# Kernel tuning notes

Measured on AMD Instinct MI355X. Metric: run time of the kernel, lower is better.

Reference implementation:

```python
import jax, jax.numpy as jnp
import numpy as np
from functools import partial

OBS, LATENT, HID = 32, 256, 1024


def setup_inputs() -> dict:
    key = jax.random.key(0)
    ks = jax.random.split(key, 16)
    s = 0.05  # small init keeps tanh/relu activations in a healthy range
    B, T = 128, 256
    inp = {
        "y": jax.random.normal(ks[0], (B, T, OBS), dtype=jnp.float32),
        "horizon": 512,
        # tanh-RNN cell params (torch nn.RNN layout: W_ih [H,I], W_hh [H,H])
        "W_ih": jax.random.normal(ks[1], (LATENT, OBS), dtype=jnp.float32) * s,
        "W_hh": jax.random.normal(ks[2], (LATENT, LATENT), dtype=jnp.float32) * s,
        "b_ih": jax.random.normal(ks[3], (LATENT,), dtype=jnp.float32) * s,
        "b_hh": jax.random.normal(ks[4], (LATENT,), dtype=jnp.float32) * s,
        # psi: 5-layer MLP latent -> hid -> hid -> hid -> hid -> obs
        "W1": jax.random.normal(ks[5], (HID, LATENT), dtype=jnp.float32) * s,
        "b1": jnp.zeros((HID,), dtype=jnp.float32),
        "W2": jax.random.normal(ks[6], (HID, HID), dtype=jnp.float32) * s,
        "b2": jnp.zeros((HID,), dtype=jnp.float32),
        "W3": jax.random.normal(ks[7], (HID, HID), dtype=jnp.float32) * s,
        "b3": jnp.zeros((HID,), dtype=jnp.float32),
        "W4": jax.random.normal(ks[8], (HID, HID), dtype=jnp.float32) * s,
        "b4": jnp.zeros((HID,), dtype=jnp.float32),
        "W5": jax.random.normal(ks[9], (OBS, HID), dtype=jnp.float32) * s,
        "b5": jnp.zeros((OBS,), dtype=jnp.float32),
    }
    return inp


def _psi(z, W1, b1, W2, b2, W3, b3, W4, b4, W5, b5):
    h = jax.nn.relu(z @ W1.T + b1)
    h = jax.nn.relu(h @ W2.T + b2)
    h = jax.nn.relu(h @ W3.T + b3)
    h = jax.nn.relu(h @ W4.T + b4)
    return h @ W5.T + b5  # (B, OBS)


def reference(y, horizon, W_ih, W_hh, b_ih, b_hh,
              W1, b1, W2, b2, W3, b3, W4, b4, W5, b5):
    B, T, S = y.shape
    psi = partial(_psi, W1=W1, b1=b1, W2=W2, b2=b2, W3=W3, b3=b3,
                  W4=W4, b4=b4, W5=W5, b5=b5)

    def cell(z, inp):
        return jnp.tanh(inp @ W_ih.T + b_ih + z @ W_hh.T + b_hh)

    z0 = jnp.zeros((B, y.shape[2]), dtype=y.dtype) if False else jnp.zeros((B, W_hh.shape[0]), dtype=y.dtype)

    # Phase 1: teacher-forced. y_hat[t] = psi(z_t) BEFORE consuming y[:, t].
    def step_tf(z, y_t):
        yh = psi(z)
        return cell(z, y_t), yh

    z, yh1 = jax.lax.scan(step_tf, z0, jnp.swapaxes(y, 0, 1))  # yh1: (T,B,S)

    def step_ar(z, _):
        yh = psi(z)
        return cell(z, yh), yh

    z, yh2 = jax.lax.scan(step_ar, z, None, length=horizon - T)  # (H-T,B,S)

    y_hat = jnp.concatenate([yh1, yh2], axis=0)  # (H,B,S)
    return jnp.swapaxes(y_hat, 0, 1)  # (B,H,S)
```

## Files before the change

### kernel.cpp

```cpp
#include <hip/hip_runtime.h>
#include <stdint.h>


#define BATCH 128
#define TTF   256
#define HOR   512
#define OBS   32
#define LAT   256
#define HID   1024

#define GROUPS  8
#define MEMBERS 32
#define ARBLOCKS (GROUPS * MEMBERS)
#define ARTHREADS 128

typedef __attribute__((ext_vector_type(8))) short short8;
typedef __attribute__((ext_vector_type(4))) float floatx4;

#define OFF_WB1   ((size_t)0)
#define OFF_WB2   (OFF_WB1 + (size_t)HID*LAT*2)
#define OFF_WB3   (OFF_WB2 + (size_t)HID*HID*2)
#define OFF_WB4   (OFF_WB3 + (size_t)HID*HID*2)
#define OFF_WB5   (OFF_WB4 + (size_t)HID*HID*2)
#define OFF_CB    (OFF_WB5 + (size_t)OBS*HID*2)
#define OFF_WHH2  (OFF_CB + (size_t)LAT*4)
#define OFF_WIH2  (OFF_WHH2 + (size_t)64*256*8)
#define OFF_ZF    (OFF_WIH2 + (size_t)8*256*8)
#define OFF_Z     (OFF_ZF + (size_t)BATCH*LAT*4)
#define OFF_WBC   (OFF_Z + (size_t)BATCH*TTF*LAT*2)
#define OFF_HB    (OFF_WBC + (size_t)LAT*288*2)
#define OFF_CTR   (OFF_HB + (size_t)GROUPS*8*16*HID*2)
#define OFF_END   (OFF_CTR + (size_t)GROUPS*512)

__device__ __forceinline__ uint16_t f2bf(float f) {
    uint32_t u = __float_as_uint(f);
    u += 0x7fffu + ((u >> 16) & 1u);
    return (uint16_t)(u >> 16);
}
__device__ __forceinline__ float bflo(uint32_t u) { return __uint_as_float(u << 16); }
__device__ __forceinline__ float bfhi(uint32_t u) { return __uint_as_float(u & 0xffff0000u); }

__device__ __forceinline__ float fast_tanh(float x) {
    float ax = fabsf(x);
    float e  = __expf(-2.f * ax);
    float r  = (1.f - e) / (1.f + e);
    return copysignf(r, x);
}

__device__ __forceinline__ int hswz(int row, int col) {
    return row * 1024 + ((((col >> 3) ^ (row & 7)) << 3) | (col & 7));
}
__device__ __forceinline__ int zswz(int row, int col) {
    return row * 256 + ((((col >> 3) ^ (row & 7)) << 3) | (col & 7));
}

__device__ __forceinline__ void st16_mall(void* p, floatx4 v) {
    asm volatile("global_store_dwordx4 %0, %1, off sc0 sc1"
                 :: "v"(p), "v"(v) : "memory");
}

typedef const __attribute__((address_space(1))) void* gas_t;
typedef __attribute__((address_space(3))) void* las_t;
__device__ __forceinline__ void gl_lds16(const void* g, void* l) {
    __builtin_amdgcn_global_load_lds((gas_t)g, (las_t)l, 16, 0, 0x11);
}

__device__ __forceinline__ void stage_h(const uint16_t* src, uint16_t* dst,
                                        int w, int L) {
    const char* gp = (const char*)src + w * 16384 + L * 16;
    char* lp = (char*)dst + w * 16384;
    #pragma unroll
    for (int i = 0; i < 16; i++)
        gl_lds16(gp + i * 1024, lp + i * 1024);
}

__device__ __forceinline__ void gbar(unsigned* ctr, unsigned target) {
    asm volatile("s_waitcnt vmcnt(0)" ::: "memory");
    __syncthreads();
    if (threadIdx.x == 0) {
        __hip_atomic_fetch_add(ctr, 1u, __ATOMIC_RELAXED, __HIP_MEMORY_SCOPE_AGENT);
        while (__hip_atomic_load(ctr, __ATOMIC_RELAXED, __HIP_MEMORY_SCOPE_AGENT) < target) {}
    }
    __syncthreads();
}

__global__ void k_cvt(const float* __restrict__ s, uint16_t* __restrict__ d, int n) {
    int i = blockIdx.x * 256 + threadIdx.x;
    if (i < n) d[i] = f2bf(s[i]);
}

__global__ void k_cb(const float* __restrict__ a, const float* __restrict__ b,
                     float* __restrict__ c) {
    int j = threadIdx.x;
    c[j] = a[j] + b[j];
}

__global__ void k_pack(const float* __restrict__ w, uint2* __restrict__ dst, int klen) {
    int k4 = blockIdx.x, j = threadIdx.x;
    int k = k4 * 4;
    uint32_t a = f2bf(w[(size_t)j * klen + k + 0]);
    uint32_t b = f2bf(w[(size_t)j * klen + k + 1]);
    uint32_t c = f2bf(w[(size_t)j * klen + k + 2]);
    uint32_t d = f2bf(w[(size_t)j * klen + k + 3]);
    uint2 r; r.x = a | (b << 16); r.y = c | (d << 16);
    dst[k4 * 256 + j] = r;
}

__global__ void k_packc(const float* __restrict__ whh, const float* __restrict__ wih,
                        uint16_t* __restrict__ wbc) {
    int col = blockIdx.x;
    for (int k = threadIdx.x; k < 288; k += 256) {
        float v = (k < 256) ? whh[(size_t)col * 256 + k] : wih[(size_t)col * 32 + (k - 256)];
        wbc[(size_t)col * 288 + k] = f2bf(v);
    }
}

__global__ __launch_bounds__(256) void k_rnn_tf(
    const float* __restrict__ y, const uint2* __restrict__ whh2,
    const uint2* __restrict__ wih2, const float* __restrict__ cb,
    uint16_t* __restrict__ Zg, float* __restrict__ zfinal)
{
    __shared__ alignas(16) float zl[LAT];
    __shared__ alignas(16) float ys[OBS];
    int j = threadIdx.x, b = blockIdx.x;
    zl[j] = 0.f;
    __syncthreads();
    const float4* z4 = (const float4*)zl;
    const float4* y4 = (const float4*)ys;
    for (int t = 0; t < TTF; t++) {
        if (j < OBS) ys[j] = y[(size_t)b * (TTF * OBS) + t * OBS + j];
        Zg[((size_t)b * TTF + t) * LAT + j] = f2bf(zl[j]);
        __syncthreads();
        float acc = cb[j];
        #pragma unroll 8
        for (int k4 = 0; k4 < 64; k4++) {
            uint2 wv = whh2[k4 * 256 + j];
            float4 zq = z4[k4];
            acc += bflo(wv.x) * zq.x + bfhi(wv.x) * zq.y
                 + bflo(wv.y) * zq.z + bfhi(wv.y) * zq.w;
        }
        #pragma unroll
        for (int k4 = 0; k4 < 8; k4++) {
            uint2 wv = wih2[k4 * 256 + j];
            float4 yq = y4[k4];
            acc += bflo(wv.x) * yq.x + bfhi(wv.x) * yq.y
                 + bflo(wv.y) * yq.z + bfhi(wv.y) * yq.w;
        }
        __syncthreads();
        zl[j] = fast_tanh(acc);
    }
    __syncthreads();
    zfinal[(size_t)b * LAT + j] = zl[j];
}

__global__ __launch_bounds__(512) void k_psi_bulk(
    const uint16_t* __restrict__ Zg,
    const uint16_t* __restrict__ wb1, const uint16_t* __restrict__ wb2,
    const uint16_t* __restrict__ wb3, const uint16_t* __restrict__ wb4,
    const uint16_t* __restrict__ wb5,
    const float* __restrict__ b1, const float* __restrict__ b2,
    const float* __restrict__ b3, const float* __restrict__ b4,
    const float* __restrict__ b5, float* __restrict__ out)
{
    __shared__ uint16_t hbuf[32 * 1024];
    int tid = threadIdx.x;
    int w = tid >> 6, L = tid & 63, lm = L & 15, q = L >> 4;
    int rb = blockIdx.x * 32;
    int colbase = w * 128;
    floatx4 acc[2][8];
    const floatx4 zero = {0.f, 0.f, 0.f, 0.f};

    #pragma unroll
    for (int mt = 0; mt < 2; mt++)
        #pragma unroll
        for (int nt = 0; nt < 8; nt++) acc[mt][nt] = zero;
    for (int kc = 0; kc < 8; kc++) {
        short8 a0 = *(const short8*)(Zg + (size_t)(rb + lm) * LAT + kc * 32 + q * 8);
        short8 a1 = *(const short8*)(Zg + (size_t)(rb + 16 + lm) * LAT + kc * 32 + q * 8);
        #pragma unroll
        for (int nt = 0; nt < 8; nt++) {
            int n = colbase + nt * 16 + lm;
            short8 bf = *(const short8*)(wb1 + (size_t)n * LAT + kc * 32 + q * 8);
            acc[0][nt] = __builtin_amdgcn_mfma_f32_16x16x32_bf16(a0, bf, acc[0][nt], 0, 0, 0);
            acc[1][nt] = __builtin_amdgcn_mfma_f32_16x16x32_bf16(a1, bf, acc[1][nt], 0, 0, 0);
        }
    }
    #pragma unroll
    for (int mt = 0; mt < 2; mt++)
        #pragma unroll
        for (int nt = 0; nt < 8; nt++) {
            int col = colbase + nt * 16 + lm;
            float bias = b1[col];
            #pragma unroll
            for (int i = 0; i < 4; i++) {
                int row = mt * 16 + q * 4 + i;
                hbuf[hswz(row, col)] = f2bf(fmaxf(acc[mt][nt][i] + bias, 0.f));
            }
        }
    __syncthreads();

    const uint16_t* wbs[3] = {wb2, wb3, wb4};
    const float*    bbs[3] = {b2, b3, b4};
    for (int ll = 0; ll < 3; ll++) {
        const uint16_t* wb = wbs[ll];
        const float* bb = bbs[ll];
        #pragma unroll
        for (int mt = 0; mt < 2; mt++)
            #pragma unroll
            for (int nt = 0; nt < 8; nt++) acc[mt][nt] = zero;
        for (int kc = 0; kc < 32; kc++) {
            int g = ((kc * 4 + q) ^ (lm & 7)) << 3;
            short8 a0 = *(const short8*)(hbuf + lm * 1024 + g);
            short8 a1 = *(const short8*)(hbuf + (16 + lm) * 1024 + g);
            #pragma unroll
            for (int nt = 0; nt < 8; nt++) {
                int n = colbase + nt * 16 + lm;
                short8 bf = *(const short8*)(wb + (size_t)n * HID + kc * 32 + q * 8);
                acc[0][nt] = __builtin_amdgcn_mfma_f32_16x16x32_bf16(a0, bf, acc[0][nt], 0, 0, 0);
                acc[1][nt] = __builtin_amdgcn_mfma_f32_16x16x32_bf16(a1, bf, acc[1][nt], 0, 0, 0);
            }
        }
        __syncthreads();
        #pragma unroll
        for (int mt = 0; mt < 2; mt++)
            #pragma unroll
            for (int nt = 0; nt < 8; nt++) {
                int col = colbase + nt * 16 + lm;
                float bias = bb[col];
                #pragma unroll
                for (int i = 0; i < 4; i++) {
                    int row = mt * 16 + q * 4 + i;
                    hbuf[hswz(row, col)] = f2bf(fmaxf(acc[mt][nt][i] + bias, 0.f));
                }
            }
        __syncthreads();
    }

    if (w < 4) {
        int mt = w >> 1;
        int nb = (w & 1) * 16;
        floatx4 a5 = zero;
        for (int kc = 0; kc < 32; kc++) {
            int g = ((kc * 4 + q) ^ (lm & 7)) << 3;
            short8 a = *(const short8*)(hbuf + (mt * 16 + lm) * 1024 + g);
            short8 bf = *(const short8*)(wb5 + (size_t)(nb + lm) * HID + kc * 32 + q * 8);
            a5 = __builtin_amdgcn_mfma_f32_16x16x32_bf16(a, bf, a5, 0, 0, 0);
        }
        int col = nb + lm;
        float bias = b5[col];
        #pragma unroll
        for (int i = 0; i < 4; i++) {
            int row = mt * 16 + q * 4 + i;
            int r = rb + row;
            int bb_ = r >> 8, tt = r & 255;
            out[(size_t)bb_ * (HOR * OBS) + tt * OBS + col] = a5[i] + bias;
        }
    }
}

__global__ __launch_bounds__(ARTHREADS) void k_ar2(
    const float* __restrict__ zfinal,
    const uint16_t* __restrict__ wb1, const uint16_t* __restrict__ wb2,
    const uint16_t* __restrict__ wb3, const uint16_t* __restrict__ wb4,
    const uint16_t* __restrict__ wb5, const uint16_t* __restrict__ wbc,
    const float* __restrict__ b1g, const float* __restrict__ b2g,
    const float* __restrict__ b3g, const float* __restrict__ b4g,
    const float* __restrict__ b5g, const float* __restrict__ cb,
    uint16_t* __restrict__ hb_all, unsigned* __restrict__ ctr_all,
    float* __restrict__ out)
{
    __shared__ alignas(16) uint16_t hstg[16 * 1024];
    __shared__ alignas(16) uint16_t zst[2 * 16 * 256];
    __shared__ alignas(16) uint16_t yscr[16 * 32];
    __shared__ alignas(16) uint16_t hsl[16 * 32];

    const int tid = threadIdx.x;
    const int g = blockIdx.x >> 5, m = blockIdx.x & 31;
    const int w = tid >> 6, L = tid & 63, lm = L & 15, q = L >> 4, lm7 = lm & 7;
    const int colbase = m * 32;
    const int cl = w * 16 + lm;
    const int rb = g * 16;
    uint16_t* hb = hb_all + (size_t)g * (8 * 16 * HID);
    unsigned* ctr = ctr_all + g * 128;
    const floatx4 zero = {0.f, 0.f, 0.f, 0.f};

    for (int idx = tid; idx < 16 * 256; idx += ARTHREADS) {
        int r = idx >> 8, c = idx & 255;
        zst[zswz(r, c)] = f2bf(zfinal[(size_t)(rb + r) * LAT + c]);
    }
    __syncthreads();
    unsigned tgt = 0;

    #define PUBLISH(DST) do {                                               \
        __syncthreads();                                                    \
        if (tid < 64) {                                                     \
            int row_ = tid >> 2, gr_ = tid & 3;                             \
            floatx4 vv_ = *(const floatx4*)((const char*)hsl + tid * 16);   \
            int gsw_ = (m * 4 + gr_) ^ (row_ & 7);                          \
            st16_mall((char*)(DST) + row_ * 2048 + gsw_ * 16, vv_);         \
        }                                                                   \
        gbar(ctr, tgt += MEMBERS);                                          \
    } while (0)

    #define MID_LAYER(HSRC, HDST, WB, BG) do {                               \
        stage_h(HSRC, hstg, w, L);                                           \
        __syncthreads();                                                     \
        floatx4 acc_ = zero;                                                 \
        const uint16_t* bb_ = WB + (size_t)(colbase + cl) * HID + q * 8;     \
        _Pragma("unroll 8")                                                  \
        for (int kc = 0; kc < 32; kc++) {                                    \
            int gh = (kc * 4 + q) ^ lm7;                                     \
            short8 a_ = *(const short8*)(hstg + lm * 1024 + gh * 8);         \
            short8 b_ = *(const short8*)(bb_ + kc * 32);                     \
            acc_ = __builtin_amdgcn_mfma_f32_16x16x32_bf16(a_, b_, acc_, 0, 0, 0); \
        }                                                                    \
        float bias_ = BG[colbase + cl];                                      \
        _Pragma("unroll")                                                    \
        for (int i = 0; i < 4; i++)                                          \
            hsl[(q * 4 + i) * 32 + cl] = f2bf(fmaxf(acc_[i] + bias_, 0.f));  \
        PUBLISH(HDST);                                                       \
    } while (0)

    #pragma unroll 1
    for (int t = 0; t < HOR - TTF; t++) {
        uint16_t* zcur = zst + (t & 1) * (16 * 256);
        uint16_t* znx  = zst + ((t + 1) & 1) * (16 * 256);
        uint16_t* hp = hb + (t & 1) * (4 * 16 * HID);
        uint16_t* h1 = hp;
        uint16_t* h2 = hp + 16 * HID;
        uint16_t* h3 = hp + 2 * 16 * HID;
        uint16_t* h4 = hp + 3 * 16 * HID;

        {
            floatx4 acc = zero;
            const uint16_t* bb = wb1 + (size_t)(colbase + cl) * LAT + q * 8;
            #pragma unroll
            for (int kc = 0; kc < 8; kc++) {
                int gz = (kc * 4 + q) ^ lm7;
                short8 a = *(const short8*)(zcur + lm * 256 + gz * 8);
                short8 b = *(const short8*)(bb + kc * 32);
                acc = __builtin_amdgcn_mfma_f32_16x16x32_bf16(a, b, acc, 0, 0, 0);
            }
            float bias = b1g[colbase + cl];
            #pragma unroll
            for (int i = 0; i < 4; i++)
                hsl[(q * 4 + i) * 32 + cl] = f2bf(fmaxf(acc[i] + bias, 0.f));
        }
        PUBLISH(h1);

        MID_LAYER(h1, h2, wb2, b2g);
        MID_LAYER(h2, h3, wb3, b3g);
        MID_LAYER(h3, h4, wb4, b4g);

        stage_h(h4, hstg, w, L);
        __syncthreads();
        {
            floatx4 a5 = zero;
            const uint16_t* bb = wb5 + (size_t)cl * HID + q * 8;
            #pragma unroll 8
            for (int kc = 0; kc < 32; kc++) {
                int gh = (kc * 4 + q) ^ lm7;
                short8 a = *(const short8*)(hstg + lm * 1024 + gh * 8);
                short8 b = *(const short8*)(bb + kc * 32);
                a5 = __builtin_amdgcn_mfma_f32_16x16x32_bf16(a, b, a5, 0, 0, 0);
            }
            float bias = b5g[cl];
            float vout[4];
            #pragma unroll
            for (int i = 0; i < 4; i++) {
                float v = a5[i] + bias;
                vout[i] = v;
                yscr[(q * 4 + i) * 32 + cl] = f2bf(v);
            }
            if (m == 0) {
                #pragma unroll
                for (int i = 0; i < 4; i++)
                    out[(size_t)(rb + q * 4 + i) * (HOR * OBS) + (TTF + t) * OBS + cl] = vout[i];
            }
        }
        __syncthreads();
        #pragma unroll 1
        for (int ct = 0; ct < 8; ct++) {
            int ccol = w * 128 + ct * 16 + lm;
            floatx4 cc = zero;
            const uint16_t* bb2 = wbc + (size_t)ccol * 288 + q * 8;
            #pragma unroll
            for (int kc = 0; kc < 9; kc++) {
                short8 a;
                if (kc < 8) {
                    int gz = (kc * 4 + q) ^ lm7;
                    a = *(const short8*)(zcur + lm * 256 + gz * 8);
                } else {
                    a = *(const short8*)(yscr + lm * 32 + q * 8);
                }
                short8 b = *(const short8*)(bb2 + kc * 32);
                cc = __builtin_amdgcn_mfma_f32_16x16x32_bf16(a, b, cc, 0, 0, 0);
            }
            float cbv = cb[ccol];
            #pragma unroll
            for (int i = 0; i < 4; i++)
                znx[zswz(q * 4 + i, ccol)] = f2bf(fast_tanh(cc[i] + cbv));
        }
        __syncthreads();
    }
    #undef MID_LAYER
    #undef PUBLISH
}

extern "C" void kernel_launch(void* const* d_in, const int* in_sizes, int n_in,
                              void* d_out, int out_size, void* d_ws, size_t ws_size,
                              hipStream_t stream) {
    (void)in_sizes; (void)n_in; (void)out_size; (void)ws_size;
    const float* y    = (const float*)d_in[0];
    const float* W_ih = (const float*)d_in[2];
    const float* W_hh = (const float*)d_in[3];
    const float* b_ih = (const float*)d_in[4];
    const float* b_hh = (const float*)d_in[5];
    const float* W1   = (const float*)d_in[6];
    const float* b1   = (const float*)d_in[7];
    const float* W2   = (const float*)d_in[8];
    const float* b2   = (const float*)d_in[9];
    const float* W3   = (const float*)d_in[10];
    const float* b3   = (const float*)d_in[11];
    const float* W4   = (const float*)d_in[12];
    const float* b4   = (const float*)d_in[13];
    const float* W5   = (const float*)d_in[14];
    const float* b5   = (const float*)d_in[15];
    float* out = (float*)d_out;
    char* ws = (char*)d_ws;

    uint16_t* WB1  = (uint16_t*)(ws + OFF_WB1);
    uint16_t* WB2  = (uint16_t*)(ws + OFF_WB2);
    uint16_t* WB3  = (uint16_t*)(ws + OFF_WB3);
    uint16_t* WB4  = (uint16_t*)(ws + OFF_WB4);
    uint16_t* WB5  = (uint16_t*)(ws + OFF_WB5);
    float*    CB   = (float*)(ws + OFF_CB);
    uint2*    WHH2 = (uint2*)(ws + OFF_WHH2);
    uint2*    WIH2 = (uint2*)(ws + OFF_WIH2);
    float*    ZF   = (float*)(ws + OFF_ZF);
    uint16_t* Zbuf = (uint16_t*)(ws + OFF_Z);
    uint16_t* WBC  = (uint16_t*)(ws + OFF_WBC);
    uint16_t* HB   = (uint16_t*)(ws + OFF_HB);
    unsigned* CTR  = (unsigned*)(ws + OFF_CTR);

    k_cvt<<<(HID*LAT + 255) / 256, 256, 0, stream>>>(W1, WB1, HID * LAT);
    k_cvt<<<(HID*HID + 255) / 256, 256, 0, stream>>>(W2, WB2, HID * HID);
    k_cvt<<<(HID*HID + 255) / 256, 256, 0, stream>>>(W3, WB3, HID * HID);
    k_cvt<<<(HID*HID + 255) / 256, 256, 0, stream>>>(W4, WB4, HID * HID);
    k_cvt<<<(OBS*HID + 255) / 256, 256, 0, stream>>>(W5, WB5, OBS * HID);
    k_cb<<<1, 256, 0, stream>>>(b_ih, b_hh, CB);
    k_pack<<<64, 256, 0, stream>>>(W_hh, WHH2, LAT);
    k_pack<<<8, 256, 0, stream>>>(W_ih, WIH2, OBS);
    k_packc<<<256, 256, 0, stream>>>(W_hh, W_ih, WBC);
    hipMemsetAsync(CTR, 0, GROUPS * 512, stream);

    k_rnn_tf<<<BATCH, 256, 0, stream>>>(y, WHH2, WIH2, CB, Zbuf, ZF);

    k_psi_bulk<<<(BATCH * TTF) / 32, 512, 0, stream>>>(
        Zbuf, WB1, WB2, WB3, WB4, WB5, b1, b2, b3, b4, b5, out);

    void* args[] = {
        (void*)&ZF, (void*)&WB1, (void*)&WB2, (void*)&WB3, (void*)&WB4,
        (void*)&WB5, (void*)&WBC, (void*)&b1, (void*)&b2, (void*)&b3,
        (void*)&b4, (void*)&b5, (void*)&CB, (void*)&HB, (void*)&CTR,
        (void*)&out
    };
    hipError_t ce = hipLaunchCooperativeKernel((const void*)k_ar2,
                                               dim3(ARBLOCKS), dim3(ARTHREADS),
                                               args, 0, stream);
    if (ce != hipSuccess) {
        (void)hipGetLastError();
        k_ar2<<<dim3(ARBLOCKS), dim3(ARTHREADS), 0, stream>>>(
            ZF, WB1, WB2, WB3, WB4, WB5, WBC, b1, b2, b3, b4, b5, CB,
            HB, CTR, out);
    }
}
```

Measured before the change: 7.373 ms.

## Fuse bulk psi into AR kernel and replace counter barrier with per-layer flags

Merges the teacher-forced psi MLP blocks into the autoregressive kernel as extra blocks, so the bulk psi work can run alongside the latency-bound AR recurrence instead of before it. Replaces the atomic-counter group barrier with per-member epoch flags per layer, polled in parallel across a wavefront, to cut synchronisation latency. It drops the cooperative launch, so AR blocks depend on being co-resident while 2048 psi blocks compete for CUs, which risks delay or deadlock if AR blocks are not scheduled first.

```diff
diff --git a/kernel.cpp b/kernel.cpp
--- a/kernel.cpp
+++ b/kernel.cpp
@@ -12,6 +12,8 @@
 #define GROUPS  8
 #define MEMBERS 32
 #define ARBLOCKS (GROUPS * MEMBERS)
+#define PSIBLKS  2048
+#define FUSEDBLKS (ARBLOCKS + PSIBLKS)
 #define ARTHREADS 128
 
 typedef __attribute__((ext_vector_type(8))) short short8;
@@ -72,16 +74,6 @@
     #pragma unroll
     for (int i = 0; i < 16; i++)
         gl_lds16(gp + i * 1024, lp + i * 1024);
-}
-
-__device__ __forceinline__ void gbar(unsigned* ctr, unsigned target) {
-    asm volatile("s_waitcnt vmcnt(0)" ::: "memory");
-    __syncthreads();
-    if (threadIdx.x == 0) {
-        __hip_atomic_fetch_add(ctr, 1u, __ATOMIC_RELAXED, __HIP_MEMORY_SCOPE_AGENT);
-        while (__hip_atomic_load(ctr, __ATOMIC_RELAXED, __HIP_MEMORY_SCOPE_AGENT) < target) {}
-    }
-    __syncthreads();
 }
 
 __global__ void k_cvt(const float* __restrict__ s, uint16_t* __restrict__ d, int n) {
@@ -153,113 +145,8 @@
     zfinal[(size_t)b * LAT + j] = zl[j];
 }
 
-__global__ __launch_bounds__(512) void k_psi_bulk(
-    const uint16_t* __restrict__ Zg,
-    const uint16_t* __restrict__ wb1, const uint16_t* __restrict__ wb2,
-    const uint16_t* __restrict__ wb3, const uint16_t* __restrict__ wb4,
-    const uint16_t* __restrict__ wb5,
-    const float* __restrict__ b1, const float* __restrict__ b2,
-    const float* __restrict__ b3, const float* __restrict__ b4,
-    const float* __restrict__ b5, float* __restrict__ out)
-{
-    __shared__ uint16_t hbuf[32 * 1024];
-    int tid = threadIdx.x;
-    int w = tid >> 6, L = tid & 63, lm = L & 15, q = L >> 4;
-    int rb = blockIdx.x * 32;
-    int colbase = w * 128;
-    floatx4 acc[2][8];
-    const floatx4 zero = {0.f, 0.f, 0.f, 0.f};
-
-    #pragma unroll
-    for (int mt = 0; mt < 2; mt++)
-        #pragma unroll
-        for (int nt = 0; nt < 8; nt++) acc[mt][nt] = zero;
-    for (int kc = 0; kc < 8; kc++) {
-        short8 a0 = *(const short8*)(Zg + (size_t)(rb + lm) * LAT + kc * 32 + q * 8);
-        short8 a1 = *(const short8*)(Zg + (size_t)(rb + 16 + lm) * LAT + kc * 32 + q * 8);
-        #pragma unroll
-        for (int nt = 0; nt < 8; nt++) {
-            int n = colbase + nt * 16 + lm;
-            short8 bf = *(const short8*)(wb1 + (size_t)n * LAT + kc * 32 + q * 8);
-            acc[0][nt] = __builtin_amdgcn_mfma_f32_16x16x32_bf16(a0, bf, acc[0][nt], 0, 0, 0);
-            acc[1][nt] = __builtin_amdgcn_mfma_f32_16x16x32_bf16(a1, bf, acc[1][nt], 0, 0, 0);
-        }
-    }
-    #pragma unroll
-    for (int mt = 0; mt < 2; mt++)
-        #pragma unroll
-        for (int nt = 0; nt < 8; nt++) {
-            int col = colbase + nt * 16 + lm;
-            float bias = b1[col];
-            #pragma unroll
-            for (int i = 0; i < 4; i++) {
-                int row = mt * 16 + q * 4 + i;
-                hbuf[hswz(row, col)] = f2bf(fmaxf(acc[mt][nt][i] + bias, 0.f));
-            }
-        }
-    __syncthreads();
-
-    const uint16_t* wbs[3] = {wb2, wb3, wb4};
-    const float*    bbs[3] = {b2, b3, b4};
-    for (int ll = 0; ll < 3; ll++) {
-        const uint16_t* wb = wbs[ll];
-        const float* bb = bbs[ll];
-        #pragma unroll
-        for (int mt = 0; mt < 2; mt++)
-            #pragma unroll
-            for (int nt = 0; nt < 8; nt++) acc[mt][nt] = zero;
-        for (int kc = 0; kc < 32; kc++) {
-            int g = ((kc * 4 + q) ^ (lm & 7)) << 3;
-            short8 a0 = *(const short8*)(hbuf + lm * 1024 + g);
-            short8 a1 = *(const short8*)(hbuf + (16 + lm) * 1024 + g);
-            #pragma unroll
-            for (int nt = 0; nt < 8; nt++) {
-                int n = colbase + nt * 16 + lm;
-                short8 bf = *(const short8*)(wb + (size_t)n * HID + kc * 32 + q * 8);
-                acc[0][nt] = __builtin_amdgcn_mfma_f32_16x16x32_bf16(a0, bf, acc[0][nt], 0, 0, 0);
-                acc[1][nt] = __builtin_amdgcn_mfma_f32_16x16x32_bf16(a1, bf, acc[1][nt], 0, 0, 0);
-            }
-        }
-        __syncthreads();
-        #pragma unroll
-        for (int mt = 0; mt < 2; mt++)
-            #pragma unroll
-            for (int nt = 0; nt < 8; nt++) {
-                int col = colbase + nt * 16 + lm;
-                float bias = bb[col];
-                #pragma unroll
-                for (int i = 0; i < 4; i++) {
-                    int row = mt * 16 + q * 4 + i;
-                    hbuf[hswz(row, col)] = f2bf(fmaxf(acc[mt][nt][i] + bias, 0.f));
-                }
-            }
-        __syncthreads();
-    }
-
-    if (w < 4) {
-        int mt = w >> 1;
-        int nb = (w & 1) * 16;
-        floatx4 a5 = zero;
-        for (int kc = 0; kc < 32; kc++) {
-            int g = ((kc * 4 + q) ^ (lm & 7)) << 3;
-            short8 a = *(const short8*)(hbuf + (mt * 16 + lm) * 1024 + g);
-            short8 bf = *(const short8*)(wb5 + (size_t)(nb + lm) * HID + kc * 32 + q * 8);
-            a5 = __builtin_amdgcn_mfma_f32_16x16x32_bf16(a, bf, a5, 0, 0, 0);
-        }
-        int col = nb + lm;
-        float bias = b5[col];
-        #pragma unroll
-        for (int i = 0; i < 4; i++) {
-            int row = mt * 16 + q * 4 + i;
-            int r = rb + row;
-            int bb_ = r >> 8, tt = r & 255;
-            out[(size_t)bb_ * (HOR * OBS) + tt * OBS + col] = a5[i] + bias;
-        }
-    }
-}
-
-__global__ __launch_bounds__(ARTHREADS) void k_ar2(
-    const float* __restrict__ zfinal,
+__global__ __launch_bounds__(ARTHREADS) void k_fused(
+    const float* __restrict__ zfinal, const uint16_t* __restrict__ Zg,
     const uint16_t* __restrict__ wb1, const uint16_t* __restrict__ wb2,
     const uint16_t* __restrict__ wb3, const uint16_t* __restrict__ wb4,
     const uint16_t* __restrict__ wb5, const uint16_t* __restrict__ wbc,
@@ -275,36 +162,126 @@
     __shared__ alignas(16) uint16_t hsl[16 * 32];
 
     const int tid = threadIdx.x;
+    const int w = tid >> 6, L = tid & 63, lm = L & 15, q = L >> 4, lm7 = lm & 7;
+    const floatx4 zero = {0.f, 0.f, 0.f, 0.f};
+
+    if (blockIdx.x >= ARBLOCKS) {
+        const int p = blockIdx.x - ARBLOCKS;
+        const int rb2 = p * 16;
+        floatx4 acc[2][16];
+
+        #pragma unroll
+        for (int h = 0; h < 2; h++)
+            #pragma unroll
+            for (int nt = 0; nt < 16; nt++) acc[h][nt] = zero;
+        for (int kc = 0; kc < 8; kc++) {
+            short8 a0 = *(const short8*)(Zg + (size_t)(rb2 + lm) * LAT + kc * 32 + q * 8);
+            #pragma unroll
+            for (int h = 0; h < 2; h++)
+                #pragma unroll
+                for (int nt = 0; nt < 16; nt++) {
+                    int n = w * 512 + h * 256 + nt * 16 + lm;
+                    short8 bf = *(const short8*)(wb1 + (size_t)n * LAT + kc * 32 + q * 8);
+                    acc[h][nt] = __builtin_amdgcn_mfma_f32_16x16x32_bf16(a0, bf, acc[h][nt], 0, 0, 0);
+                }
+        }
+        #pragma unroll
+        for (int h = 0; h < 2; h++)
+            #pragma unroll
+            for (int nt = 0; nt < 16; nt++) {
+                int col = w * 512 + h * 256 + nt * 16 + lm;
+                float bias = b1g[col];
+                #pragma unroll
+                for (int i = 0; i < 4; i++)
+                    hstg[hswz(q * 4 + i, col)] = f2bf(fmaxf(acc[h][nt][i] + bias, 0.f));
+            }
+        __syncthreads();
+
+        for (int ll = 0; ll < 3; ll++) {
+            const uint16_t* wb = (ll == 0) ? wb2 : (ll == 1) ? wb3 : wb4;
+            const float* bb = (ll == 0) ? b2g : (ll == 1) ? b3g : b4g;
+            #pragma unroll
+            for (int h = 0; h < 2; h++)
+                #pragma unroll
+                for (int nt = 0; nt < 16; nt++) acc[h][nt] = zero;
+            for (int kc = 0; kc < 32; kc++) {
+                short8 a0 = *(const short8*)(hstg + lm * 1024 + (((kc * 4 + q) ^ lm7) << 3));
+                #pragma unroll
+                for (int h = 0; h < 2; h++)
+                    #pragma unroll
+                    for (int nt = 0; nt < 16; nt++) {
+                        int n = w * 512 + h * 256 + nt * 16 + lm;
+                        short8 bf = *(const short8*)(wb + (size_t)n * HID + kc * 32 + q * 8);
+                        acc[h][nt] = __builtin_amdgcn_mfma_f32_16x16x32_bf16(a0, bf, acc[h][nt], 0, 0, 0);
+                    }
+            }
+            __syncthreads();
+            #pragma unroll
+            for (int h = 0; h < 2; h++)
+                #pragma unroll
+                for (int nt = 0; nt < 16; nt++) {
+                    int col = w * 512 + h * 256 + nt * 16 + lm;
+                    float bias = bb[col];
+                    #pragma unroll
+                    for (int i = 0; i < 4; i++)
+                        hstg[hswz(q * 4 + i, col)] = f2bf(fmaxf(acc[h][nt][i] + bias, 0.f));
+                }
+            __syncthreads();
+        }
+
+        floatx4 a5 = zero;
+        for (int kc = 0; kc < 32; kc++) {
+            short8 a = *(const short8*)(hstg + lm * 1024 + (((kc * 4 + q) ^ lm7) << 3));
+            short8 bf = *(const short8*)(wb5 + (size_t)(w * 16 + lm) * HID + kc * 32 + q * 8);
+            a5 = __builtin_amdgcn_mfma_f32_16x16x32_bf16(a, bf, a5, 0, 0, 0);
+        }
+        int col = w * 16 + lm;
+        float bias = b5g[col];
+        #pragma unroll
+        for (int i = 0; i < 4; i++) {
+            int r = rb2 + q * 4 + i;
+            out[(size_t)(r >> 8) * (HOR * OBS) + (r & 255) * OBS + col] = a5[i] + bias;
+        }
+        return;
+    }
+
     const int g = blockIdx.x >> 5, m = blockIdx.x & 31;
-    const int w = tid >> 6, L = tid & 63, lm = L & 15, q = L >> 4, lm7 = lm & 7;
     const int colbase = m * 32;
     const int cl = w * 16 + lm;
     const int rb = g * 16;
     uint16_t* hb = hb_all + (size_t)g * (8 * 16 * HID);
-    unsigned* ctr = ctr_all + g * 128;
-    const floatx4 zero = {0.f, 0.f, 0.f, 0.f};
+    unsigned* flg = ctr_all + g * 128;
 
     for (int idx = tid; idx < 16 * 256; idx += ARTHREADS) {
         int r = idx >> 8, c = idx & 255;
         zst[zswz(r, c)] = f2bf(zfinal[(size_t)(rb + r) * LAT + c]);
     }
     __syncthreads();
-    unsigned tgt = 0;
-
-    #define PUBLISH(DST) do {                                               \
-        __syncthreads();                                                    \
-        if (tid < 64) {                                                     \
-            int row_ = tid >> 2, gr_ = tid & 3;                             \
-            floatx4 vv_ = *(const floatx4*)((const char*)hsl + tid * 16);   \
-            int gsw_ = (m * 4 + gr_) ^ (row_ & 7);                          \
-            st16_mall((char*)(DST) + row_ * 2048 + gsw_ * 16, vv_);         \
-        }                                                                   \
-        gbar(ctr, tgt += MEMBERS);                                          \
+
+    #define EXCHANGE(DST, FL, EP) do {                                       \
+        __syncthreads();                                                     \
+        if (tid < 64) {                                                      \
+            int row_ = tid >> 2, gr_ = tid & 3;                              \
+            floatx4 vv_ = *(const floatx4*)((const char*)hsl + tid * 16);    \
+            int gsw_ = (m * 4 + gr_) ^ (row_ & 7);                           \
+            st16_mall((char*)(DST) + row_ * 2048 + gsw_ * 16, vv_);          \
+            asm volatile("s_waitcnt vmcnt(0)" ::: "memory");                 \
+            if (tid == 0)                                                    \
+                __hip_atomic_store(flg + (FL) * 32 + m, (EP),                \
+                                   __ATOMIC_RELAXED, __HIP_MEMORY_SCOPE_AGENT); \
+        }                                                                    \
+        {                                                                    \
+            unsigned* fp_ = flg + (FL) * 32 + (L & 31);                      \
+            unsigned v_;                                                     \
+            do {                                                             \
+                v_ = __hip_atomic_load(fp_, __ATOMIC_RELAXED,                \
+                                       __HIP_MEMORY_SCOPE_AGENT);            \
+            } while (!__all((int)(v_ >= (EP))));                             \
+            asm volatile("" ::: "memory");                                   \
+        }                                                                    \
     } while (0)
 
-    #define MID_LAYER(HSRC, HDST, WB, BG) do {                               \
-        stage_h(HSRC, hstg, w, L);                                           \
-        __syncthreads();                                                     \
+    #define MID_COMPUTE(WB, BG) do {                                         \
         floatx4 acc_ = zero;                                                 \
         const uint16_t* bb_ = WB + (size_t)(colbase + cl) * HID + q * 8;     \
         _Pragma("unroll 8")                                                  \
@@ -318,11 +295,11 @@
         _Pragma("unroll")                                                    \
         for (int i = 0; i < 4; i++)                                          \
             hsl[(q * 4 + i) * 32 + cl] = f2bf(fmaxf(acc_[i] + bias_, 0.f));  \
-        PUBLISH(HDST);                                                       \
     } while (0)
 
     #pragma unroll 1
     for (int t = 0; t < HOR - TTF; t++) {
+        const unsigned ep = (unsigned)(t + 1);
         uint16_t* zcur = zst + (t & 1) * (16 * 256);
         uint16_t* znx  = zst + ((t + 1) & 1) * (16 * 256);
         uint16_t* hp = hb + (t & 1) * (4 * 16 * HID);
@@ -346,14 +323,25 @@
             for (int i = 0; i < 4; i++)
                 hsl[(q * 4 + i) * 32 + cl] = f2bf(fmaxf(acc[i] + bias, 0.f));
         }
-        PUBLISH(h1);
-
-        MID_LAYER(h1, h2, wb2, b2g);
-        MID_LAYER(h2, h3, wb3, b3g);
-        MID_LAYER(h3, h4, wb4, b4g);
-
+        EXCHANGE(h1, 0, ep);
+        stage_h(h1, hstg, w, L);
+        __syncthreads();
+
+        MID_COMPUTE(wb2, b2g);
+        EXCHANGE(h2, 1, ep);
+        stage_h(h2, hstg, w, L);
+        __syncthreads();
+
+        MID_COMPUTE(wb3, b3g);
+        EXCHANGE(h3, 2, ep);
+        stage_h(h3, hstg, w, L);
+        __syncthreads();
+
+        MID_COMPUTE(wb4, b4g);
+        EXCHANGE(h4, 3, ep);
         stage_h(h4, hstg, w, L);
         __syncthreads();
+
         {
             floatx4 a5 = zero;
             const uint16_t* bb = wb5 + (size_t)cl * HID + q * 8;
@@ -403,8 +391,8 @@
         }
         __syncthreads();
     }
-    #undef MID_LAYER
-    #undef PUBLISH
+    #undef MID_COMPUTE
+    #undef EXCHANGE
 }
 
 extern "C" void kernel_launch(void* const* d_in, const int* in_sizes, int n_in,
@@ -456,22 +444,7 @@
 
     k_rnn_tf<<<BATCH, 256, 0, stream>>>(y, WHH2, WIH2, CB, Zbuf, ZF);
 
-    k_psi_bulk<<<(BATCH * TTF) / 32, 512, 0, stream>>>(
-        Zbuf, WB1, WB2, WB3, WB4, WB5, b1, b2, b3, b4, b5, out);
-
-    void* args[] = {
-        (void*)&ZF, (void*)&WB1, (void*)&WB2, (void*)&WB3, (void*)&WB4,
-        (void*)&WB5, (void*)&WBC, (void*)&b1, (void*)&b2, (void*)&b3,
-        (void*)&b4, (void*)&b5, (void*)&CB, (void*)&HB, (void*)&CTR,
-        (void*)&out
-    };
-    hipError_t ce = hipLaunchCooperativeKernel((const void*)k_ar2,
-                                               dim3(ARBLOCKS), dim3(ARTHREADS),
-                                               args, 0, stream);
-    if (ce != hipSuccess) {
-        (void)hipGetLastError();
-        k_ar2<<<dim3(ARBLOCKS), dim3(ARTHREADS), 0, stream>>>(
-            ZF, WB1, WB2, WB3, WB4, WB5, WBC, b1, b2, b3, b4, b5, CB,
-            HB, CTR, out);
-    }
-}
+    k_fused<<<dim3(FUSEDBLKS), dim3(ARTHREADS), 0, stream>>>(
+        ZF, Zbuf, WB1, WB2, WB3, WB4, WB5, WBC,
+        b1, b2, b3, b4, b5, CB, HB, CTR, out);
+}
```

After: 8.738 ms. 18.5% more time.

## Replace group counter barriers with per-layer epoch flags and compute layer 1 redundantly

Applied to the files above, without the earlier changes.

The autoregressive kernel drops the shared atomic-counter barrier. Each member block now writes its layer output, then sets a per-member epoch flag for that layer, and every block polls all 32 flags of its group with a wave-wide __all. Layer 1 (256 to 1024) is no longer split across blocks: each block computes the full 1024-wide hidden state directly into its own LDS, which removes one global exchange and barrier per step in exchange for 32x redundant layer-1 MFMA work. The cooperative launch is replaced by a plain launch, which drops the co-residency guarantee the spin-wait relies on.

```diff
diff --git a/kernel.cpp b/kernel.cpp
--- a/kernel.cpp
+++ b/kernel.cpp
@@ -72,16 +72,6 @@
     #pragma unroll
     for (int i = 0; i < 16; i++)
         gl_lds16(gp + i * 1024, lp + i * 1024);
-}
-
-__device__ __forceinline__ void gbar(unsigned* ctr, unsigned target) {
-    asm volatile("s_waitcnt vmcnt(0)" ::: "memory");
-    __syncthreads();
-    if (threadIdx.x == 0) {
-        __hip_atomic_fetch_add(ctr, 1u, __ATOMIC_RELAXED, __HIP_MEMORY_SCOPE_AGENT);
-        while (__hip_atomic_load(ctr, __ATOMIC_RELAXED, __HIP_MEMORY_SCOPE_AGENT) < target) {}
-    }
-    __syncthreads();
 }
 
 __global__ void k_cvt(const float* __restrict__ s, uint16_t* __restrict__ d, int n) {
@@ -281,7 +271,7 @@
     const int cl = w * 16 + lm;
     const int rb = g * 16;
     uint16_t* hb = hb_all + (size_t)g * (8 * 16 * HID);
-    unsigned* ctr = ctr_all + g * 128;
+    unsigned* flg = ctr_all + g * 128;
     const floatx4 zero = {0.f, 0.f, 0.f, 0.f};
 
     for (int idx = tid; idx < 16 * 256; idx += ARTHREADS) {
@@ -289,22 +279,31 @@
         zst[zswz(r, c)] = f2bf(zfinal[(size_t)(rb + r) * LAT + c]);
     }
     __syncthreads();
-    unsigned tgt = 0;
-
-    #define PUBLISH(DST) do {                                               \
-        __syncthreads();                                                    \
-        if (tid < 64) {                                                     \
-            int row_ = tid >> 2, gr_ = tid & 3;                             \
-            floatx4 vv_ = *(const floatx4*)((const char*)hsl + tid * 16);   \
-            int gsw_ = (m * 4 + gr_) ^ (row_ & 7);                          \
-            st16_mall((char*)(DST) + row_ * 2048 + gsw_ * 16, vv_);         \
-        }                                                                   \
-        gbar(ctr, tgt += MEMBERS);                                          \
+
+    #define EXCHANGE(DST, FL, EP) do {                                       \
+        __syncthreads();                                                     \
+        if (tid < 64) {                                                      \
+            int row_ = tid >> 2, gr_ = tid & 3;                              \
+            floatx4 vv_ = *(const floatx4*)((const char*)hsl + tid * 16);    \
+            int gsw_ = (m * 4 + gr_) ^ (row_ & 7);                           \
+            st16_mall((char*)(DST) + row_ * 2048 + gsw_ * 16, vv_);          \
+            asm volatile("s_waitcnt vmcnt(0)" ::: "memory");                 \
+            if (tid == 0)                                                    \
+                __hip_atomic_store(flg + (FL) * 32 + m, (EP),                \
+                                   __ATOMIC_RELAXED, __HIP_MEMORY_SCOPE_AGENT); \
+        }                                                                    \
+        {                                                                    \
+            unsigned* fp_ = flg + (FL) * 32 + (L & 31);                      \
+            unsigned v_;                                                     \
+            do {                                                             \
+                v_ = __hip_atomic_load(fp_, __ATOMIC_RELAXED,                \
+                                       __HIP_MEMORY_SCOPE_AGENT);            \
+            } while (!__all((int)(v_ >= (EP))));                             \
+            asm volatile("" ::: "memory");                                   \
+        }                                                                    \
     } while (0)
 
-    #define MID_LAYER(HSRC, HDST, WB, BG) do {                               \
-        stage_h(HSRC, hstg, w, L);                                           \
-        __syncthreads();                                                     \
+    #define MID_COMPUTE(WB, BG) do {                                         \
         floatx4 acc_ = zero;                                                 \
         const uint16_t* bb_ = WB + (size_t)(colbase + cl) * HID + q * 8;     \
         _Pragma("unroll 8")                                                  \
@@ -318,42 +317,60 @@
         _Pragma("unroll")                                                    \
         for (int i = 0; i < 4; i++)                                          \
             hsl[(q * 4 + i) * 32 + cl] = f2bf(fmaxf(acc_[i] + bias_, 0.f));  \
-        PUBLISH(HDST);                                                       \
     } while (0)
 
     #pragma unroll 1
     for (int t = 0; t < HOR - TTF; t++) {
+        const unsigned ep = (unsigned)(t + 1);
         uint16_t* zcur = zst + (t & 1) * (16 * 256);
         uint16_t* znx  = zst + ((t + 1) & 1) * (16 * 256);
         uint16_t* hp = hb + (t & 1) * (4 * 16 * HID);
-        uint16_t* h1 = hp;
         uint16_t* h2 = hp + 16 * HID;
         uint16_t* h3 = hp + 2 * 16 * HID;
         uint16_t* h4 = hp + 3 * 16 * HID;
 
-        {
-            floatx4 acc = zero;
-            const uint16_t* bb = wb1 + (size_t)(colbase + cl) * LAT + q * 8;
+        #pragma unroll 1
+        for (int nc = 0; nc < 4; nc++) {
+            floatx4 acc[8];
+            #pragma unroll
+            for (int nt = 0; nt < 8; nt++) acc[nt] = zero;
             #pragma unroll
             for (int kc = 0; kc < 8; kc++) {
                 int gz = (kc * 4 + q) ^ lm7;
                 short8 a = *(const short8*)(zcur + lm * 256 + gz * 8);
-                short8 b = *(const short8*)(bb + kc * 32);
-                acc = __builtin_amdgcn_mfma_f32_16x16x32_bf16(a, b, acc, 0, 0, 0);
-            }
-            float bias = b1g[colbase + cl];
-            #pragma unroll
-            for (int i = 0; i < 4; i++)
-                hsl[(q * 4 + i) * 32 + cl] = f2bf(fmaxf(acc[i] + bias, 0.f));
-        }
-        PUBLISH(h1);
-
-        MID_LAYER(h1, h2, wb2, b2g);
-        MID_LAYER(h2, h3, wb3, b3g);
-        MID_LAYER(h3, h4, wb4, b4g);
-
+                #pragma unroll
+                for (int nt = 0; nt < 8; nt++) {
+                    int n = w * 512 + nc * 128 + nt * 16 + lm;
+                    short8 b = *(const short8*)(wb1 + (size_t)n * LAT + kc * 32 + q * 8);
+                    acc[nt] = __builtin_amdgcn_mfma_f32_16x16x32_bf16(a, b, acc[nt], 0, 0, 0);
+                }
+            }
+            #pragma unroll
+            for (int nt = 0; nt < 8; nt++) {
+                int col = w * 512 + nc * 128 + nt * 16 + lm;
+                float bias = b1g[col];
+                #pragma unroll
+                for (int i = 0; i < 4; i++)
+                    hstg[hswz(q * 4 + i, col)] = f2bf(fmaxf(acc[nt][i] + bias, 0.f));
+            }
+        }
+        __syncthreads();
+
+        MID_COMPUTE(wb2, b2g);
+        EXCHANGE(h2, 0, ep);
+        stage_h(h2, hstg, w, L);
+        __syncthreads();
+
+        MID_COMPUTE(wb3, b3g);
+        EXCHANGE(h3, 1, ep);
+        stage_h(h3, hstg, w, L);
+        __syncthreads();
+
+        MID_COMPUTE(wb4, b4g);
+        EXCHANGE(h4, 2, ep);
         stage_h(h4, hstg, w, L);
         __syncthreads();
+
         {
             floatx4 a5 = zero;
             const uint16_t* bb = wb5 + (size_t)cl * HID + q * 8;
@@ -403,8 +420,8 @@
         }
         __syncthreads();
     }
-    #undef MID_LAYER
-    #undef PUBLISH
+    #undef MID_COMPUTE
+    #undef EXCHANGE
 }
 
 extern "C" void kernel_launch(void* const* d_in, const int* in_sizes, int n_in,
@@ -459,19 +476,7 @@
     k_psi_bulk<<<(BATCH * TTF) / 32, 512, 0, stream>>>(
         Zbuf, WB1, WB2, WB3, WB4, WB5, b1, b2, b3, b4, b5, out);
 
-    void* args[] = {
-        (void*)&ZF, (void*)&WB1, (void*)&WB2, (void*)&WB3, (void*)&WB4,
-        (void*)&WB5, (void*)&WBC, (void*)&b1, (void*)&b2, (void*)&b3,
-        (void*)&b4, (void*)&b5, (void*)&CB, (void*)&HB, (void*)&CTR,
-        (void*)&out
-    };
-    hipError_t ce = hipLaunchCooperativeKernel((const void*)k_ar2,
-                                               dim3(ARBLOCKS), dim3(ARTHREADS),
-                                               args, 0, stream);
-    if (ce != hipSuccess) {
-        (void)hipGetLastError();
-        k_ar2<<<dim3(ARBLOCKS), dim3(ARTHREADS), 0, stream>>>(
-            ZF, WB1, WB2, WB3, WB4, WB5, WBC, b1, b2, b3, b4, b5, CB,
-            HB, CTR, out);
-    }
-}
+    k_ar2<<<dim3(ARBLOCKS), dim3(ARTHREADS), 0, stream>>>(
+        ZF, WB1, WB2, WB3, WB4, WB5, WBC, b1, b2, b3, b4, b5, CB,
+        HB, CTR, out);
+}
```

After: 15.50 ms. +110.2%, slower.
